# Optimization experiments

Measured on AMD Instinct MI355X. Metric: run time of the kernel, lower is better.

## Reference

```python
import jax, jax.numpy as jnp
import numpy as np

QMAX = 255.0  # uint8 range used by KVQuantizer


def setup_inputs() -> dict:
    key = jax.random.key(0)
    k1, k2 = jax.random.split(key)
    B, KVH, D, S = 1, 8, 128, 8192
    keys = jax.random.normal(k1, (B, KVH, 1, D, S), dtype=jnp.float32)
    values = jax.random.normal(k2, (B, KVH, 1, S, D), dtype=jnp.float32)
    return {"keys": keys, "values": values, "mask": 1, "ids_len": S, "kv_seq_len": S}


def _quantize_block(x, axis):
    # torch.aminmax(x, dim=axis, keepdim=True)
    block_min = jnp.min(x, axis=axis, keepdims=True)
    block_max = jnp.max(x, axis=axis, keepdims=True)
    scale = (block_max - block_min) * (1.0 / QMAX)
    x_packed = jnp.round((x - block_min) / scale)  # F16 path: stays float
    # USE_FLOAT16_SCALE_BIAS=True -> half precision scale/bias
    return x_packed, scale.astype(jnp.float16), block_min.astype(jnp.float16)


def reference(keys, values, mask, ids_len, kv_seq_len):
    # causal mask: (1 - tril(ones)) * -128, sliced [:ids_len, :kv_seq_len], * mask, .float()
    row = jnp.arange(ids_len)[:, None]
    col = jnp.arange(kv_seq_len)[None, :]
    attn = (jnp.where(col > row, jnp.int32(-128), jnp.int32(0)) * jnp.int32(mask)).astype(jnp.float32)
    attn = attn[None, None, None]  # [1,1,1,ids_len,kv_seq_len]

    # per-layer KV-cache quantization (keys blocked over head_dim axis -2, values over -1)
    k_packed, k_scale, k_bias = _quantize_block(keys, -2)
    v_packed, v_scale, v_bias = _quantize_block(values, -1)
    return (attn, k_packed, k_scale, k_bias, v_packed, jnp.swapaxes(v_scale, -1, -2), v_bias)
```

## Files before the change

### kernel.cpp

```cpp
#include <hip/hip_runtime.h>
#include <hip/hip_fp16.h>

#define HH 8
#define DD 128
#define SS 8192

__global__ __launch_bounds__(256) void attn_kernel(const int* __restrict__ maskp,
                                                   float* __restrict__ out) {
    const float hi = (float)(-128 * (*maskp));
    int idx = blockIdx.x * 256 + threadIdx.x;
    int r  = idx >> 11;
    int c  = (idx & 2047) << 2;
    float4 v;
    v.x = (c + 0 > r) ? hi : 0.0f;
    v.y = (c + 1 > r) ? hi : 0.0f;
    v.z = (c + 2 > r) ? hi : 0.0f;
    v.w = (c + 3 > r) ? hi : 0.0f;
    ((float4*)out)[idx] = v;
}

__global__ __launch_bounds__(256) void keys_kernel(const float* __restrict__ keys,
                                                   float* __restrict__ kp,
                                                   float* __restrict__ ks,
                                                   float* __restrict__ kb) {
    const int h  = blockIdx.x >> 7;
    const int s0 = (blockIdx.x & 127) << 6;
    const int sl = threadIdx.x & 63;
    const int td = threadIdx.x >> 6;

    const float* base = keys + (size_t)h * DD * SS + s0 + sl;
    float val[32];
    float mn = 3.0e38f, mx = -3.0e38f;
#pragma unroll
    for (int j = 0; j < 32; ++j) {
        float v = base[(size_t)(td * 32 + j) * SS];
        val[j] = v;
        mn = fminf(mn, v);
        mx = fmaxf(mx, v);
    }

    __shared__ float smin[4][64], smax[4][64], sscale[64], sbias[64];
    smin[td][sl] = mn;
    smax[td][sl] = mx;
    __syncthreads();
    if (td == 0) {
        float m0 = fminf(fminf(smin[0][sl], smin[1][sl]), fminf(smin[2][sl], smin[3][sl]));
        float M0 = fmaxf(fmaxf(smax[0][sl], smax[1][sl]), fmaxf(smax[2][sl], smax[3][sl]));
        float scale = (M0 - m0) * (1.0f / 255.0f);
        sscale[sl] = scale;
        sbias[sl]  = m0;
        int o = h * SS + s0 + sl;
        ks[o] = __half2float(__float2half(scale));
        kb[o] = __half2float(__float2half(m0));
    }
    __syncthreads();
    const float scale = sscale[sl];
    const float bias  = sbias[sl];
    float* ob = kp + (size_t)h * DD * SS + s0 + sl;
#pragma unroll
    for (int j = 0; j < 32; ++j) {
        ob[(size_t)(td * 32 + j) * SS] = rintf((val[j] - bias) / scale);
    }
}

__global__ __launch_bounds__(256) void vals_kernel(const float* __restrict__ vals,
                                                   float* __restrict__ vp,
                                                   float* __restrict__ vs,
                                                   float* __restrict__ vb) {
    const int d4 = threadIdx.x & 31;
    const int rr = threadIdx.x >> 5;
    const int R  = blockIdx.x * 8 + rr;

    const float4 v = ((const float4*)vals)[R * 32 + d4];
    float mn = fminf(fminf(v.x, v.y), fminf(v.z, v.w));
    float mx = fmaxf(fmaxf(v.x, v.y), fmaxf(v.z, v.w));
#pragma unroll
    for (int off = 16; off >= 1; off >>= 1) {
        mn = fminf(mn, __shfl_xor(mn, off));
        mx = fmaxf(mx, __shfl_xor(mx, off));
    }
    const float scale = (mx - mn) * (1.0f / 255.0f);
    if (d4 == 0) {
        vs[R] = __half2float(__float2half(scale));
        vb[R] = __half2float(__float2half(mn));
    }
    float4 o;
    o.x = rintf((v.x - mn) / scale);
    o.y = rintf((v.y - mn) / scale);
    o.z = rintf((v.z - mn) / scale);
    o.w = rintf((v.w - mn) / scale);
    ((float4*)vp)[R * 32 + d4] = o;
}

extern "C" void kernel_launch(void* const* d_in, const int* in_sizes, int n_in,
                              void* d_out, int out_size, void* d_ws, size_t ws_size,
                              hipStream_t stream) {
    const float* keys  = (const float*)d_in[0];
    const float* vals  = (const float*)d_in[1];
    const int*   maskp = (const int*)d_in[2];

    float* out  = (float*)d_out;
    float* attn = out;
    float* kp   = attn + 67108864;
    float* ks   = kp   + 8388608;
    float* kb   = ks   + 65536;
    float* vp   = kb   + 65536;
    float* vs   = vp   + 8388608;
    float* vb   = vs   + 65536;

    attn_kernel<<<dim3(SS * (SS / 4) / 256), dim3(256), 0, stream>>>(maskp, attn);
    keys_kernel<<<dim3(HH * (SS / 64)), dim3(256), 0, stream>>>(keys, kp, ks, kb);
    vals_kernel<<<dim3(HH * SS / 8), dim3(256), 0, stream>>>(vals, vp, vs, vb);
}
```

Measured before the change: 373.2 us.

## Fuse attn, keys and values quantization into one launch with vectorized stores

Merges the three kernels into a single 512-thread kernel that dispatches on block index, so key and value quantization run alongside the large causal-mask fill. The keys path now loads and stores float4 columns, and both quantization paths replace the per-element divide with a reciprocal multiply. The mask fill writes eight float4s per thread with nontemporal stores. The reciprocal multiply may round differently from true division in rare cases.

```diff
diff --git a/kernel.cpp b/kernel.cpp
--- a/kernel.cpp
+++ b/kernel.cpp
@@ -5,91 +5,130 @@
 #define DD 128
 #define SS 8192
 
-__global__ __launch_bounds__(256) void attn_kernel(const int* __restrict__ maskp,
-                                                   float* __restrict__ out) {
-    const float hi = (float)(-128 * (*maskp));
-    int idx = blockIdx.x * 256 + threadIdx.x;
-    int r  = idx >> 11;
-    int c  = (idx & 2047) << 2;
-    float4 v;
-    v.x = (c + 0 > r) ? hi : 0.0f;
-    v.y = (c + 1 > r) ? hi : 0.0f;
-    v.z = (c + 2 > r) ? hi : 0.0f;
-    v.w = (c + 3 > r) ? hi : 0.0f;
-    ((float4*)out)[idx] = v;
-}
+#define KEYS_BLOCKS 256
+#define VALS_BLOCKS 4096
+#define ATTN_BLOCKS 4096
 
-__global__ __launch_bounds__(256) void keys_kernel(const float* __restrict__ keys,
-                                                   float* __restrict__ kp,
-                                                   float* __restrict__ ks,
-                                                   float* __restrict__ kb) {
-    const int h  = blockIdx.x >> 7;
-    const int s0 = (blockIdx.x & 127) << 6;
-    const int sl = threadIdx.x & 63;
-    const int td = threadIdx.x >> 6;
+typedef float nfloat4 __attribute__((ext_vector_type(4)));
 
-    const float* base = keys + (size_t)h * DD * SS + s0 + sl;
-    float val[32];
-    float mn = 3.0e38f, mx = -3.0e38f;
+__global__ __launch_bounds__(512) void fused_kernel(
+    const float* __restrict__ keys, const float* __restrict__ vals,
+    const int* __restrict__ maskp,
+    float* __restrict__ attn, float* __restrict__ kp, float* __restrict__ ks,
+    float* __restrict__ kb, float* __restrict__ vp, float* __restrict__ vs,
+    float* __restrict__ vbias)
+{
+    const int bid = blockIdx.x;
+    const int tid = threadIdx.x;
+
+    __shared__ float4 smin[8][64], smax[8][64];
+    __shared__ float4 sbias[64], sinv[64];
+
+    if (bid < KEYS_BLOCKS) {
+        const int h   = bid >> 5;
+        const int s04 = (bid & 31) << 6;
+        const int l   = tid & 63;
+        const int w   = tid >> 6;
+        const float4* k4 = (const float4*)keys;
+
+        float4 val[16];
+        float4 mn4 = make_float4(3e38f, 3e38f, 3e38f, 3e38f);
+        float4 mx4 = make_float4(-3e38f, -3e38f, -3e38f, -3e38f);
 #pragma unroll
-    for (int j = 0; j < 32; ++j) {
-        float v = base[(size_t)(td * 32 + j) * SS];
-        val[j] = v;
-        mn = fminf(mn, v);
-        mx = fmaxf(mx, v);
+        for (int j = 0; j < 16; ++j) {
+            float4 v = k4[(size_t)(h * DD + w * 16 + j) * (SS / 4) + s04 + l];
+            val[j] = v;
+            mn4.x = fminf(mn4.x, v.x); mn4.y = fminf(mn4.y, v.y);
+            mn4.z = fminf(mn4.z, v.z); mn4.w = fminf(mn4.w, v.w);
+            mx4.x = fmaxf(mx4.x, v.x); mx4.y = fmaxf(mx4.y, v.y);
+            mx4.z = fmaxf(mx4.z, v.z); mx4.w = fmaxf(mx4.w, v.w);
+        }
+        smin[w][l] = mn4;
+        smax[w][l] = mx4;
+        __syncthreads();
+        if (w == 0) {
+            float4 m = smin[0][l], M = smax[0][l];
+#pragma unroll
+            for (int i = 1; i < 8; ++i) {
+                float4 a = smin[i][l], b = smax[i][l];
+                m.x = fminf(m.x, a.x); m.y = fminf(m.y, a.y);
+                m.z = fminf(m.z, a.z); m.w = fminf(m.w, a.w);
+                M.x = fmaxf(M.x, b.x); M.y = fmaxf(M.y, b.y);
+                M.z = fmaxf(M.z, b.z); M.w = fmaxf(M.w, b.w);
+            }
+            float4 sc;
+            sc.x = (M.x - m.x) * (1.0f / 255.0f); sc.y = (M.y - m.y) * (1.0f / 255.0f);
+            sc.z = (M.z - m.z) * (1.0f / 255.0f); sc.w = (M.w - m.w) * (1.0f / 255.0f);
+            float4 kso, kbo;
+            kso.x = __half2float(__float2half(sc.x)); kso.y = __half2float(__float2half(sc.y));
+            kso.z = __half2float(__float2half(sc.z)); kso.w = __half2float(__float2half(sc.w));
+            kbo.x = __half2float(__float2half(m.x)); kbo.y = __half2float(__float2half(m.y));
+            kbo.z = __half2float(__float2half(m.z)); kbo.w = __half2float(__float2half(m.w));
+            ((float4*)ks)[h * (SS / 4) + s04 + l] = kso;
+            ((float4*)kb)[h * (SS / 4) + s04 + l] = kbo;
+            float4 inv;
+            inv.x = 1.0f / sc.x; inv.y = 1.0f / sc.y;
+            inv.z = 1.0f / sc.z; inv.w = 1.0f / sc.w;
+            sbias[l] = m;
+            sinv[l]  = inv;
+        }
+        __syncthreads();
+        const float4 b4 = sbias[l];
+        const float4 i4 = sinv[l];
+        float4* o4 = (float4*)kp;
+#pragma unroll
+        for (int j = 0; j < 16; ++j) {
+            float4 o;
+            o.x = rintf((val[j].x - b4.x) * i4.x);
+            o.y = rintf((val[j].y - b4.y) * i4.y);
+            o.z = rintf((val[j].z - b4.z) * i4.z);
+            o.w = rintf((val[j].w - b4.w) * i4.w);
+            o4[(size_t)(h * DD + w * 16 + j) * (SS / 4) + s04 + l] = o;
+        }
+    } else if (bid < KEYS_BLOCKS + VALS_BLOCKS) {
+        const int vbd = bid - KEYS_BLOCKS;
+        const int d4  = tid & 31;
+        const int rr  = tid >> 5;
+        const int R   = vbd * 16 + rr;
+
+        const float4 v = ((const float4*)vals)[R * 32 + d4];
+        float mn = fminf(fminf(v.x, v.y), fminf(v.z, v.w));
+        float mx = fmaxf(fmaxf(v.x, v.y), fmaxf(v.z, v.w));
+#pragma unroll
+        for (int off = 16; off >= 1; off >>= 1) {
+            mn = fminf(mn, __shfl_xor(mn, off));
+            mx = fmaxf(mx, __shfl_xor(mx, off));
+        }
+        const float scale = (mx - mn) * (1.0f / 255.0f);
+        const float inv = 1.0f / scale;
+        if (d4 == 0) {
+            vs[R]    = __half2float(__float2half(scale));
+            vbias[R] = __half2float(__float2half(mn));
+        }
+        float4 o;
+        o.x = rintf((v.x - mn) * inv);
+        o.y = rintf((v.y - mn) * inv);
+        o.z = rintf((v.z - mn) * inv);
+        o.w = rintf((v.w - mn) * inv);
+        ((float4*)vp)[R * 32 + d4] = o;
+    } else {
+        const int ab = bid - (KEYS_BLOCKS + VALS_BLOCKS);
+        const float hi = (float)(-128 * (*maskp));
+        const int base = ab * 4096 + tid;
+        nfloat4* o4 = (nfloat4*)attn;
+#pragma unroll
+        for (int k2 = 0; k2 < 8; ++k2) {
+            int idx = base + k2 * 512;
+            int r = idx >> 11;
+            int c = (idx & 2047) << 2;
+            nfloat4 v;
+            v.x = (c + 0 > r) ? hi : 0.0f;
+            v.y = (c + 1 > r) ? hi : 0.0f;
+            v.z = (c + 2 > r) ? hi : 0.0f;
+            v.w = (c + 3 > r) ? hi : 0.0f;
+            __builtin_nontemporal_store(v, &o4[idx]);
+        }
     }
-
-    __shared__ float smin[4][64], smax[4][64], sscale[64], sbias[64];
-    smin[td][sl] = mn;
-    smax[td][sl] = mx;
-    __syncthreads();
-    if (td == 0) {
-        float m0 = fminf(fminf(smin[0][sl], smin[1][sl]), fminf(smin[2][sl], smin[3][sl]));
-        float M0 = fmaxf(fmaxf(smax[0][sl], smax[1][sl]), fmaxf(smax[2][sl], smax[3][sl]));
-        float scale = (M0 - m0) * (1.0f / 255.0f);
-        sscale[sl] = scale;
-        sbias[sl]  = m0;
-        int o = h * SS + s0 + sl;
-        ks[o] = __half2float(__float2half(scale));
-        kb[o] = __half2float(__float2half(m0));
-    }
-    __syncthreads();
-    const float scale = sscale[sl];
-    const float bias  = sbias[sl];
-    float* ob = kp + (size_t)h * DD * SS + s0 + sl;
-#pragma unroll
-    for (int j = 0; j < 32; ++j) {
-        ob[(size_t)(td * 32 + j) * SS] = rintf((val[j] - bias) / scale);
-    }
-}
-
-__global__ __launch_bounds__(256) void vals_kernel(const float* __restrict__ vals,
-                                                   float* __restrict__ vp,
-                                                   float* __restrict__ vs,
-                                                   float* __restrict__ vb) {
-    const int d4 = threadIdx.x & 31;
-    const int rr = threadIdx.x >> 5;
-    const int R  = blockIdx.x * 8 + rr;
-
-    const float4 v = ((const float4*)vals)[R * 32 + d4];
-    float mn = fminf(fminf(v.x, v.y), fminf(v.z, v.w));
-    float mx = fmaxf(fmaxf(v.x, v.y), fmaxf(v.z, v.w));
-#pragma unroll
-    for (int off = 16; off >= 1; off >>= 1) {
-        mn = fminf(mn, __shfl_xor(mn, off));
-        mx = fmaxf(mx, __shfl_xor(mx, off));
-    }
-    const float scale = (mx - mn) * (1.0f / 255.0f);
-    if (d4 == 0) {
-        vs[R] = __half2float(__float2half(scale));
-        vb[R] = __half2float(__float2half(mn));
-    }
-    float4 o;
-    o.x = rintf((v.x - mn) / scale);
-    o.y = rintf((v.y - mn) / scale);
-    o.z = rintf((v.z - mn) / scale);
-    o.w = rintf((v.w - mn) / scale);
-    ((float4*)vp)[R * 32 + d4] = o;
 }
 
 extern "C" void kernel_launch(void* const* d_in, const int* in_sizes, int n_in,
@@ -106,9 +145,9 @@
     float* kb   = ks   + 65536;
     float* vp   = kb   + 65536;
     float* vs   = vp   + 8388608;
-    float* vb   = vs   + 65536;
+    float* vbv  = vs   + 65536;
 
-    attn_kernel<<<dim3(SS * (SS / 4) / 256), dim3(256), 0, stream>>>(maskp, attn);
-    keys_kernel<<<dim3(HH * (SS / 64)), dim3(256), 0, stream>>>(keys, kp, ks, kb);
-    vals_kernel<<<dim3(HH * SS / 8), dim3(256), 0, stream>>>(vals, vp, vs, vb);
+    const int grid = KEYS_BLOCKS + VALS_BLOCKS + ATTN_BLOCKS;
+    fused_kernel<<<dim3(grid), dim3(512), 0, stream>>>(
+        keys, vals, maskp, attn, kp, ks, kb, vp, vs, vbv);
 }
```

New measurement: 384.2 us. 2.9% more time.
